# Performance work log

Hardware: AMD Instinct MI355X
Metric: run time of the kernel (lower is better)

## Reference

```python
import jax, jax.numpy as jnp
import numpy as np

B, H, K, V = 64, 32, 128, 128


def setup_inputs() -> dict:
    key = jax.random.key(0)
    ks = jax.random.split(key, 7)
    q = jax.random.normal(ks[0], (B, 1, H, K), dtype=jnp.float32)
    k = jax.random.normal(ks[1], (B, 1, H, K), dtype=jnp.float32)
    v = jax.random.normal(ks[2], (B, 1, H, V), dtype=jnp.float32)
    # a = -kappa, b = kappa*a_gate in RWKV-7; plain gaussians suffice for a math reference
    a = jax.random.normal(ks[3], (B, 1, H, K), dtype=jnp.float32)
    b = jax.random.normal(ks[4], (B, 1, H, K), dtype=jnp.float32)
    # gk is a log-decay: negative so exp(gk) in (0, 1]
    gk = -jnp.abs(jax.random.normal(ks[5], (B, 1, H, K), dtype=jnp.float32)) * 0.1
    h0 = jax.random.normal(ks[6], (B, H, K, V), dtype=jnp.float32) * 0.1
    return {"q": q, "k": k, "v": v, "a": a, "b": b, "gk": gk, "h0": h0}


def reference(q, k, v, a, b, gk, h0):
    """RWKV-7 DPLR single-step (T=1) decode recurrence, per (batch, head):
      g     = exp(gk)                                # [K] decay
      s     = a^T H0                                 # [V]
      t     = (q*g)^T H0                             # [V]
      alpha = q . b ; beta = q . k                   # scalars
      o     = t + alpha*s + beta*v                   # [V]
      Ht    = diag(g) H0 + b s^T + k v^T             # [K,V]
    Mirrors dplr_decode_t1_kernel_streamK exactly (fp32 accumulation).
    """
    qf = q[:, 0].astype(jnp.float32)   # [B,H,K]
    kf = k[:, 0].astype(jnp.float32)
    af = a[:, 0].astype(jnp.float32)
    bf = b[:, 0].astype(jnp.float32)
    vf = v[:, 0].astype(jnp.float32)   # [B,H,V]
    g = jnp.exp(gk[:, 0].astype(jnp.float32))  # [B,H,K]
    hf = h0.astype(jnp.float32)        # [B,H,K,V]

    s = jnp.einsum('bhk,bhkv->bhv', af, hf)
    t = jnp.einsum('bhk,bhkv->bhv', qf * g, hf)
    alpha = jnp.sum(qf * bf, axis=-1, keepdims=True)  # [B,H,1]
    beta = jnp.sum(qf * kf, axis=-1, keepdims=True)   # [B,H,1]
    o = t + alpha * s + beta * vf                      # [B,H,V]

    ht = g[..., None] * hf + bf[..., None] * s[:, :, None, :] + kf[..., None] * vf[:, :, None, :]
    return o[:, None].astype(v.dtype), ht.astype(h0.dtype)
```

## Files before the change

kernel.cpp:

```cpp
#include <hip/hip_runtime.h>


#define KD 128
#define VD 128
#define BH_TOTAL 2048
#define NGRP 16
#define RPT 8

typedef float f32x4 __attribute__((ext_vector_type(4)));

__global__ __launch_bounds__(512, 4) void dplr_decode_t1_kernel(
    const float* __restrict__ q_,  const float* __restrict__ k_,
    const float* __restrict__ v_,  const float* __restrict__ a_,
    const float* __restrict__ b_,  const float* __restrict__ gk_,
    const float* __restrict__ h0_, float* __restrict__ out_)
{
    const int bh  = blockIdx.x;
    const int tid = threadIdx.x;
    const int c4  = (tid & 31) * 4;
    const int grp = tid >> 5;
    const int r0  = grp * RPT;

    const size_t vec_off = (size_t)bh * KD;
    const size_t h_off   = (size_t)bh * (KD * VD);

    __shared__ float qs[KD], ks[KD], bs[KD], as_[KD], gs[KD], qgs[KD], vs[VD];
    __shared__ float sred[NGRP][VD];
    __shared__ float tred[NGRP][VD];
    __shared__ float red2[2];

    f32x4 Hreg[RPT];
    const float* hp = h0_ + h_off + (size_t)r0 * VD + c4;
#pragma unroll
    for (int j = 0; j < RPT; ++j) {
        Hreg[j] = *(const f32x4*)(hp + (size_t)j * VD);
    }

    const f32x4 v4 = *(const f32x4*)(v_ + vec_off + c4);

    if (tid < KD) {
        float qq = q_[vec_off + tid];
        float gg = expf(gk_[vec_off + tid]);
        qs[tid]  = qq;
        ks[tid]  = k_[vec_off + tid];
        bs[tid]  = b_[vec_off + tid];
        as_[tid] = a_[vec_off + tid];
        gs[tid]  = gg;
        qgs[tid] = qq * gg;
        vs[tid]  = v_[vec_off + tid];
    }

#pragma unroll
    for (int j = 0; j < RPT; ++j) {
        asm volatile("" : "+v"(Hreg[j]));
    }
    __syncthreads();

    if (tid < 64) {
        float p = qs[tid] * bs[tid] + qs[tid + 64] * bs[tid + 64];
#pragma unroll
        for (int o = 32; o > 0; o >>= 1) p += __shfl_down(p, o, 64);
        if (tid == 0) red2[0] = p;
    } else if (tid < 128) {
        int l = tid - 64;
        float p = qs[l] * ks[l] + qs[l + 64] * ks[l + 64];
#pragma unroll
        for (int o = 32; o > 0; o >>= 1) p += __shfl_down(p, o, 64);
        if (l == 0) red2[1] = p;
    }

    f32x4 sp = {0.f, 0.f, 0.f, 0.f};
    f32x4 tp = {0.f, 0.f, 0.f, 0.f};
#pragma unroll
    for (int j = 0; j < RPT; ++j) {
        const float av = as_[r0 + j];
        const float qg = qgs[r0 + j];
        const f32x4 h = Hreg[j];
        sp += av * h;
        tp += qg * h;
    }
    *(f32x4*)&sred[grp][c4] = sp;
    *(f32x4*)&tred[grp][c4] = tp;
    __syncthreads();

    f32x4 s4 = {0.f, 0.f, 0.f, 0.f};
#pragma unroll
    for (int g = 0; g < NGRP; ++g) {
        s4 += *(const f32x4*)&sred[g][c4];
    }

    if (tid < VD) {
        float sc = 0.f, tc = 0.f;
#pragma unroll
        for (int g = 0; g < NGRP; ++g) { sc += sred[g][tid]; tc += tred[g][tid]; }
        out_[(size_t)bh * VD + tid] = tc + red2[0] * sc + red2[1] * vs[tid];
    }

    float* op = out_ + (size_t)BH_TOTAL * VD + h_off + (size_t)r0 * VD + c4;
#pragma unroll
    for (int j = 0; j < RPT; ++j) {
        const int r = r0 + j;
        const float gr = gs[r];
        const float br = bs[r];
        const float kr = ks[r];
        f32x4 o4 = gr * Hreg[j] + br * s4 + kr * v4;
        __builtin_nontemporal_store(o4, (f32x4*)(op + (size_t)j * VD));
    }
}

extern "C" void kernel_launch(void* const* d_in, const int* in_sizes, int n_in,
                              void* d_out, int out_size, void* d_ws, size_t ws_size,
                              hipStream_t stream) {
    const float* q  = (const float*)d_in[0];
    const float* k  = (const float*)d_in[1];
    const float* v  = (const float*)d_in[2];
    const float* a  = (const float*)d_in[3];
    const float* b  = (const float*)d_in[4];
    const float* gk = (const float*)d_in[5];
    const float* h0 = (const float*)d_in[6];
    float* out = (float*)d_out;

    dplr_decode_t1_kernel<<<BH_TOTAL, 512, 0, stream>>>(q, k, v, a, b, gk, h0, out);
}
```

Measured before the change: 254.3 us.

## Make blocks persistent over four heads with double-buffered H prefetch

The grid shrinks from one block per (batch, head) to 512 blocks, and each block processes four consecutive heads. The next head's H tile and vectors are loaded into a second register set and shared buffer while the current head is reduced and written, so global loads overlap with compute and stores. This trades lower block count and parallelism for latency hiding. It also doubles H register usage, which may pressure occupancy under launch_bounds(512,4).

```diff
diff --git a/kernel.cpp b/kernel.cpp
--- a/kernel.cpp
+++ b/kernel.cpp
@@ -6,8 +6,18 @@
 #define BH_TOTAL 2048
 #define NGRP 16
 #define RPT 8
+#define GRID 512
+#define ITERS 4
 
 typedef float f32x4 __attribute__((ext_vector_type(4)));
+
+#define LDS_BARRIER()                                      \
+    do {                                                   \
+        asm volatile("s_waitcnt lgkmcnt(0)" ::: "memory"); \
+        __builtin_amdgcn_s_barrier();                      \
+        __builtin_amdgcn_sched_barrier(0);                 \
+        asm volatile("" ::: "memory");                     \
+    } while (0)
 
 __global__ __launch_bounds__(512, 4) void dplr_decode_t1_kernel(
     const float* __restrict__ q_,  const float* __restrict__ k_,
@@ -15,97 +25,117 @@
     const float* __restrict__ b_,  const float* __restrict__ gk_,
     const float* __restrict__ h0_, float* __restrict__ out_)
 {
-    const int bh  = blockIdx.x;
     const int tid = threadIdx.x;
     const int c4  = (tid & 31) * 4;
     const int grp = tid >> 5;
     const int r0  = grp * RPT;
+    const int bh0 = blockIdx.x * ITERS;
 
-    const size_t vec_off = (size_t)bh * KD;
-    const size_t h_off   = (size_t)bh * (KD * VD);
-
-    __shared__ float qs[KD], ks[KD], bs[KD], as_[KD], gs[KD], qgs[KD], vs[VD];
+    __shared__ float qs[2][KD], ks[2][KD], bs[2][KD], as_[2][KD],
+                     gs[2][KD], qgs[2][KD], vs[2][KD];
     __shared__ float sred[NGRP][VD];
     __shared__ float tred[NGRP][VD];
     __shared__ float red2[2];
 
-    f32x4 Hreg[RPT];
-    const float* hp = h0_ + h_off + (size_t)r0 * VD + c4;
-#pragma unroll
-    for (int j = 0; j < RPT; ++j) {
-        Hreg[j] = *(const f32x4*)(hp + (size_t)j * VD);
-    }
+    f32x4 Ha[RPT], Hb[RPT];
 
-    const f32x4 v4 = *(const f32x4*)(v_ + vec_off + c4);
+    float sq = 0.f, sk = 0.f, sb = 0.f, sa = 0.f, sg = 0.f, sv = 0.f;
 
-    if (tid < KD) {
-        float qq = q_[vec_off + tid];
-        float gg = expf(gk_[vec_off + tid]);
-        qs[tid]  = qq;
-        ks[tid]  = k_[vec_off + tid];
-        bs[tid]  = b_[vec_off + tid];
-        as_[tid] = a_[vec_off + tid];
-        gs[tid]  = gg;
-        qgs[tid] = qq * gg;
-        vs[tid]  = v_[vec_off + tid];
-    }
+#define STAGE_LOAD(bh)                                   \
+    do { if (tid < KD) {                                 \
+        const size_t off = (size_t)(bh)*KD + tid;        \
+        sq = q_[off];  sk = k_[off];  sb = b_[off];      \
+        sa = a_[off];  sg = gk_[off]; sv = v_[off];      \
+    } } while (0)
 
-#pragma unroll
-    for (int j = 0; j < RPT; ++j) {
-        asm volatile("" : "+v"(Hreg[j]));
-    }
-    __syncthreads();
+#define STAGE_WRITE(p)                                   \
+    do { if (tid < KD) {                                 \
+        const float gg = expf(sg);                       \
+        qs[p][tid]  = sq;  ks[p][tid] = sk;              \
+        bs[p][tid]  = sb;  as_[p][tid] = sa;             \
+        gs[p][tid]  = gg;  qgs[p][tid] = sq * gg;        \
+        vs[p][tid]  = sv;                                \
+    } } while (0)
 
-    if (tid < 64) {
-        float p = qs[tid] * bs[tid] + qs[tid + 64] * bs[tid + 64];
-#pragma unroll
-        for (int o = 32; o > 0; o >>= 1) p += __shfl_down(p, o, 64);
-        if (tid == 0) red2[0] = p;
-    } else if (tid < 128) {
-        int l = tid - 64;
-        float p = qs[l] * ks[l] + qs[l + 64] * ks[l + 64];
-#pragma unroll
-        for (int o = 32; o > 0; o >>= 1) p += __shfl_down(p, o, 64);
-        if (l == 0) red2[1] = p;
-    }
+#define LOAD_H(H, bh)                                                     \
+    do {                                                                  \
+        const float* hp_ = h0_ + (size_t)(bh)*(KD*VD) + (size_t)r0*VD + c4; \
+        _Pragma("unroll")                                                 \
+        for (int j = 0; j < RPT; ++j)                                     \
+            H[j] = *(const f32x4*)(hp_ + (size_t)j * VD);                 \
+    } while (0)
 
-    f32x4 sp = {0.f, 0.f, 0.f, 0.f};
-    f32x4 tp = {0.f, 0.f, 0.f, 0.f};
-#pragma unroll
-    for (int j = 0; j < RPT; ++j) {
-        const float av = as_[r0 + j];
-        const float qg = qgs[r0 + j];
-        const f32x4 h = Hreg[j];
-        sp += av * h;
-        tp += qg * h;
-    }
-    *(f32x4*)&sred[grp][c4] = sp;
-    *(f32x4*)&tred[grp][c4] = tp;
-    __syncthreads();
+    STAGE_LOAD(bh0);
+    STAGE_WRITE(0);
+    LOAD_H(Ha, bh0);
+    LDS_BARRIER();
 
-    f32x4 s4 = {0.f, 0.f, 0.f, 0.f};
-#pragma unroll
-    for (int g = 0; g < NGRP; ++g) {
-        s4 += *(const f32x4*)&sred[g][c4];
-    }
+#define ITER_BODY(i, HCUR, HNXT)                                              \
+    do {                                                                      \
+        const int p = (i) & 1;                                                \
+           \
+        if ((i) + 1 < ITERS) STAGE_LOAD(bh0 + (i) + 1);                       \
+                               \
+        if (tid < 64) {                                                       \
+            float pr = qs[p][tid]*bs[p][tid] + qs[p][tid+64]*bs[p][tid+64];   \
+            _Pragma("unroll")                                                 \
+            for (int o = 32; o > 0; o >>= 1) pr += __shfl_down(pr, o, 64);    \
+            if (tid == 0) red2[0] = pr;                                       \
+        } else if (tid < 128) {                                               \
+            const int l = tid - 64;                                           \
+            float pr = qs[p][l]*ks[p][l] + qs[p][l+64]*ks[p][l+64];           \
+            _Pragma("unroll")                                                 \
+            for (int o = 32; o > 0; o >>= 1) pr += __shfl_down(pr, o, 64);    \
+            if (l == 0) red2[1] = pr;                                         \
+        }                                                                     \
+                                              \
+        f32x4 sp = {0.f,0.f,0.f,0.f}, tp = {0.f,0.f,0.f,0.f};                 \
+        _Pragma("unroll")                                                     \
+        for (int j = 0; j < RPT; ++j) {                                       \
+            const float av = as_[p][r0+j];                                    \
+            const float qg = qgs[p][r0+j];                                    \
+            sp += av * HCUR[j];                                               \
+            tp += qg * HCUR[j];                                               \
+        }                                                                     \
+        *(f32x4*)&sred[grp][c4] = sp;                                         \
+        *(f32x4*)&tred[grp][c4] = tp;                                         \
+          \
+        if ((i) + 1 < ITERS) {                                                \
+            STAGE_WRITE(p ^ 1);                                               \
+            LOAD_H(HNXT, bh0 + (i) + 1);                                      \
+        }                                                                     \
+        LDS_BARRIER();       \
+                 \
+        f32x4 s4 = {0.f,0.f,0.f,0.f};                                         \
+        _Pragma("unroll")                                                     \
+        for (int g = 0; g < NGRP; ++g) s4 += *(const f32x4*)&sred[g][c4];     \
+        const f32x4 v4 = *(const f32x4*)&vs[p][c4];                           \
+        float* op = out_ + (size_t)BH_TOTAL * VD                              \
+                  + (size_t)(bh0+(i))*(KD*VD) + (size_t)r0*VD + c4;           \
+        _Pragma("unroll")                                                     \
+        for (int j = 0; j < RPT; ++j) {                                       \
+            const int r = r0 + j;                                             \
+            f32x4 o4 = gs[p][r]*HCUR[j] + bs[p][r]*s4 + ks[p][r]*v4;          \
+            __builtin_nontemporal_store(o4, (f32x4*)(op + (size_t)j*VD));     \
+        }                                                                     \
+        if (tid < VD) {                                                       \
+            float sc = 0.f, tc = 0.f;                                         \
+            _Pragma("unroll")                                                 \
+            for (int g = 0; g < NGRP; ++g) { sc += sred[g][tid]; tc += tred[g][tid]; } \
+            out_[(size_t)(bh0+(i))*VD + tid] = tc + red2[0]*sc + red2[1]*vs[p][tid];   \
+        }                                                                     \
+        LDS_BARRIER();           \
+    } while (0)
 
-    if (tid < VD) {
-        float sc = 0.f, tc = 0.f;
-#pragma unroll
-        for (int g = 0; g < NGRP; ++g) { sc += sred[g][tid]; tc += tred[g][tid]; }
-        out_[(size_t)bh * VD + tid] = tc + red2[0] * sc + red2[1] * vs[tid];
-    }
+    ITER_BODY(0, Ha, Hb);
+    ITER_BODY(1, Hb, Ha);
+    ITER_BODY(2, Ha, Hb);
+    ITER_BODY(3, Hb, Ha);
 
-    float* op = out_ + (size_t)BH_TOTAL * VD + h_off + (size_t)r0 * VD + c4;
-#pragma unroll
-    for (int j = 0; j < RPT; ++j) {
-        const int r = r0 + j;
-        const float gr = gs[r];
-        const float br = bs[r];
-        const float kr = ks[r];
-        f32x4 o4 = gr * Hreg[j] + br * s4 + kr * v4;
-        __builtin_nontemporal_store(o4, (f32x4*)(op + (size_t)j * VD));
-    }
+#undef ITER_BODY
+#undef LOAD_H
+#undef STAGE_WRITE
+#undef STAGE_LOAD
 }
 
 extern "C" void kernel_launch(void* const* d_in, const int* in_sizes, int n_in,
@@ -120,5 +150,5 @@
     const float* h0 = (const float*)d_in[6];
     float* out = (float*)d_out;
 
-    dplr_decode_t1_kernel<<<BH_TOTAL, 512, 0, stream>>>(q, k, v, a, b, gk, h0, out);
+    dplr_decode_t1_kernel<<<GRID, 512, 0, stream>>>(q, k, v, a, b, gk, h0, out);
 }
```

New measurement: 251.6 us. Within noise of the previous version (-1.1%).

## Split fused decode into separate reduce and update kernels via workspace

Applied to the files above, without the earlier changes.

Replaces the single fused kernel with two kernels when a workspace is available. The first computes s, t and the output vector and writes s to the workspace. The second rereads H0 and writes the updated state. This removes the need to hold H in registers across a block-wide reduction and barrier, but H0 (128 MiB) is now read twice and a second launch is added. The fused kernel remains as a fallback when no workspace is provided.

```diff
diff --git a/kernel.cpp b/kernel.cpp
--- a/kernel.cpp
+++ b/kernel.cpp
@@ -4,12 +4,115 @@
 #define KD 128
 #define VD 128
 #define BH_TOTAL 2048
-#define NGRP 16
-#define RPT 8
 
 typedef float f32x4 __attribute__((ext_vector_type(4)));
 
-__global__ __launch_bounds__(512, 4) void dplr_decode_t1_kernel(
+__global__ __launch_bounds__(256) void dplr_reduce_kernel(
+    const float* __restrict__ q_,  const float* __restrict__ k_,
+    const float* __restrict__ v_,  const float* __restrict__ a_,
+    const float* __restrict__ b_,  const float* __restrict__ gk_,
+    const float* __restrict__ h0_, float* __restrict__ out_,
+    float* __restrict__ s_ws)
+{
+    const int bh  = blockIdx.x;
+    const int tid = threadIdx.x;
+    const int c4  = (tid & 31) * 4;
+    const int grp = tid >> 5;
+    const int r0  = grp * 16;
+    const size_t vec_off = (size_t)bh * KD;
+
+    __shared__ float qs[KD], ks[KD], bs[KD], as_[KD], qgs[KD];
+    __shared__ float sred[8][VD], tred[8][VD];
+    __shared__ float red2[2];
+
+    float vv = 0.f;
+    if (tid < KD) {
+        const float qq = q_[vec_off + tid];
+        const float gg = expf(gk_[vec_off + tid]);
+        qs[tid]  = qq;
+        ks[tid]  = k_[vec_off + tid];
+        bs[tid]  = b_[vec_off + tid];
+        as_[tid] = a_[vec_off + tid];
+        qgs[tid] = qq * gg;
+        vv       = v_[vec_off + tid];
+    }
+    __syncthreads();
+
+    if (tid < 64) {
+        float p = qs[tid] * bs[tid] + qs[tid + 64] * bs[tid + 64];
+#pragma unroll
+        for (int o = 32; o > 0; o >>= 1) p += __shfl_down(p, o, 64);
+        if (tid == 0) red2[0] = p;
+    } else if (tid < 128) {
+        const int l = tid - 64;
+        float p = qs[l] * ks[l] + qs[l + 64] * ks[l + 64];
+#pragma unroll
+        for (int o = 32; o > 0; o >>= 1) p += __shfl_down(p, o, 64);
+        if (l == 0) red2[1] = p;
+    }
+
+    f32x4 sp = {0.f, 0.f, 0.f, 0.f};
+    f32x4 tp = {0.f, 0.f, 0.f, 0.f};
+    const float* hp = h0_ + (size_t)bh * (KD * VD) + (size_t)r0 * VD + c4;
+#pragma unroll
+    for (int j = 0; j < 16; ++j) {
+        const f32x4 h = *(const f32x4*)(hp + (size_t)j * VD);
+        sp += as_[r0 + j] * h;
+        tp += qgs[r0 + j] * h;
+    }
+    *(f32x4*)&sred[grp][c4] = sp;
+    *(f32x4*)&tred[grp][c4] = tp;
+    __syncthreads();
+
+    if (tid < VD) {
+        float sc = 0.f, tc = 0.f;
+#pragma unroll
+        for (int g = 0; g < 8; ++g) { sc += sred[g][tid]; tc += tred[g][tid]; }
+        out_[(size_t)bh * VD + tid] = tc + red2[0] * sc + red2[1] * vv;
+        s_ws[(size_t)bh * VD + tid] = sc;
+    }
+}
+
+__global__ __launch_bounds__(256) void dplr_update_kernel(
+    const float* __restrict__ k_,  const float* __restrict__ v_,
+    const float* __restrict__ b_,  const float* __restrict__ gk_,
+    const float* __restrict__ h0_, const float* __restrict__ s_ws,
+    float* __restrict__ out_)
+{
+    const int bh  = blockIdx.x;
+    const int tid = threadIdx.x;
+    const int c4  = (tid & 31) * 4;
+    const int grp = tid >> 5;
+    const int r0  = grp * 16;
+    const size_t vec_off = (size_t)bh * KD;
+
+    __shared__ float ks[KD], bs[KD], gs[KD], vs[KD], ss[KD];
+
+    if (tid < KD) {
+        ks[tid] = k_[vec_off + tid];
+        bs[tid] = b_[vec_off + tid];
+        gs[tid] = expf(gk_[vec_off + tid]);
+        vs[tid] = v_[vec_off + tid];
+        ss[tid] = s_ws[vec_off + tid];
+    }
+    __syncthreads();
+
+    const f32x4 s4 = *(const f32x4*)&ss[c4];
+    const f32x4 v4 = *(const f32x4*)&vs[c4];
+    const float* hp = h0_ + (size_t)bh * (KD * VD) + (size_t)r0 * VD + c4;
+    float* op = out_ + (size_t)BH_TOTAL * VD
+              + (size_t)bh * (KD * VD) + (size_t)r0 * VD + c4;
+
+#pragma unroll
+    for (int j = 0; j < 16; ++j) {
+        const int r = r0 + j;
+        const f32x4 h = *(const f32x4*)(hp + (size_t)j * VD);
+        f32x4 o4 = gs[r] * h + bs[r] * s4 + ks[r] * v4;
+        __builtin_nontemporal_store(o4, (f32x4*)(op + (size_t)j * VD));
+    }
+}
+
+__global__ __launch_bounds__(512, 4) void dplr_fused_kernel(
     const float* __restrict__ q_,  const float* __restrict__ k_,
     const float* __restrict__ v_,  const float* __restrict__ a_,
     const float* __restrict__ b_,  const float* __restrict__ gk_,
@@ -19,41 +122,32 @@
     const int tid = threadIdx.x;
     const int c4  = (tid & 31) * 4;
     const int grp = tid >> 5;
-    const int r0  = grp * RPT;
+    const int r0  = grp * 8;
 
     const size_t vec_off = (size_t)bh * KD;
     const size_t h_off   = (size_t)bh * (KD * VD);
 
-    __shared__ float qs[KD], ks[KD], bs[KD], as_[KD], gs[KD], qgs[KD], vs[VD];
-    __shared__ float sred[NGRP][VD];
-    __shared__ float tred[NGRP][VD];
+    __shared__ float qs[KD], ks[KD], bs[KD], as_[KD], gs[KD], qgs[KD], vs[KD];
+    __shared__ float sred[16][VD];
+    __shared__ float tred[16][VD];
     __shared__ float red2[2];
 
-    f32x4 Hreg[RPT];
+    f32x4 Hreg[8];
     const float* hp = h0_ + h_off + (size_t)r0 * VD + c4;
 #pragma unroll
-    for (int j = 0; j < RPT; ++j) {
-        Hreg[j] = *(const f32x4*)(hp + (size_t)j * VD);
-    }
+    for (int j = 0; j < 8; ++j) Hreg[j] = *(const f32x4*)(hp + (size_t)j * VD);
 
     const f32x4 v4 = *(const f32x4*)(v_ + vec_off + c4);
 
     if (tid < KD) {
         float qq = q_[vec_off + tid];
         float gg = expf(gk_[vec_off + tid]);
-        qs[tid]  = qq;
-        ks[tid]  = k_[vec_off + tid];
-        bs[tid]  = b_[vec_off + tid];
-        as_[tid] = a_[vec_off + tid];
-        gs[tid]  = gg;
-        qgs[tid] = qq * gg;
-        vs[tid]  = v_[vec_off + tid];
-    }
-
-#pragma unroll
-    for (int j = 0; j < RPT; ++j) {
-        asm volatile("" : "+v"(Hreg[j]));
-    }
+        qs[tid]  = qq;  ks[tid]  = k_[vec_off + tid];
+        bs[tid]  = b_[vec_off + tid];  as_[tid] = a_[vec_off + tid];
+        gs[tid]  = gg;  qgs[tid] = qq * gg;  vs[tid] = v_[vec_off + tid];
+    }
+#pragma unroll
+    for (int j = 0; j < 8; ++j) asm volatile("" : "+v"(Hreg[j]));
     __syncthreads();
 
     if (tid < 64) {
@@ -69,41 +163,32 @@
         if (l == 0) red2[1] = p;
     }
 
-    f32x4 sp = {0.f, 0.f, 0.f, 0.f};
-    f32x4 tp = {0.f, 0.f, 0.f, 0.f};
-#pragma unroll
-    for (int j = 0; j < RPT; ++j) {
-        const float av = as_[r0 + j];
-        const float qg = qgs[r0 + j];
-        const f32x4 h = Hreg[j];
-        sp += av * h;
-        tp += qg * h;
+    f32x4 sp = {0.f,0.f,0.f,0.f}, tp = {0.f,0.f,0.f,0.f};
+#pragma unroll
+    for (int j = 0; j < 8; ++j) {
+        sp += as_[r0 + j] * Hreg[j];
+        tp += qgs[r0 + j] * Hreg[j];
     }
     *(f32x4*)&sred[grp][c4] = sp;
     *(f32x4*)&tred[grp][c4] = tp;
     __syncthreads();
 
-    f32x4 s4 = {0.f, 0.f, 0.f, 0.f};
-#pragma unroll
-    for (int g = 0; g < NGRP; ++g) {
-        s4 += *(const f32x4*)&sred[g][c4];
-    }
+    f32x4 s4 = {0.f,0.f,0.f,0.f};
+#pragma unroll
+    for (int g = 0; g < 16; ++g) s4 += *(const f32x4*)&sred[g][c4];
 
     if (tid < VD) {
         float sc = 0.f, tc = 0.f;
 #pragma unroll
-        for (int g = 0; g < NGRP; ++g) { sc += sred[g][tid]; tc += tred[g][tid]; }
-        out_[(size_t)bh * VD + tid] = tc + red2[0] * sc + red2[1] * vs[tid];
+        for (int g = 0; g < 16; ++g) { sc += sred[g][tid]; tc += tred[g][tid]; }
+        out_[(size_t)bh * VD + tid] = tc + red2[0]*sc + red2[1]*vs[tid];
     }
 
     float* op = out_ + (size_t)BH_TOTAL * VD + h_off + (size_t)r0 * VD + c4;
 #pragma unroll
-    for (int j = 0; j < RPT; ++j) {
+    for (int j = 0; j < 8; ++j) {
         const int r = r0 + j;
-        const float gr = gs[r];
-        const float br = bs[r];
-        const float kr = ks[r];
-        f32x4 o4 = gr * Hreg[j] + br * s4 + kr * v4;
+        f32x4 o4 = gs[r]*Hreg[j] + bs[r]*s4 + ks[r]*v4;
         __builtin_nontemporal_store(o4, (f32x4*)(op + (size_t)j * VD));
     }
 }
@@ -120,5 +205,12 @@
     const float* h0 = (const float*)d_in[6];
     float* out = (float*)d_out;
 
-    dplr_decode_t1_kernel<<<BH_TOTAL, 512, 0, stream>>>(q, k, v, a, b, gk, h0, out);
-}
+    const size_t need = (size_t)BH_TOTAL * VD * sizeof(float);
+    if (d_ws != nullptr && ws_size >= need) {
+        float* s_ws = (float*)d_ws;
+        dplr_reduce_kernel<<<BH_TOTAL, 256, 0, stream>>>(q, k, v, a, b, gk, h0, out, s_ws);
+        dplr_update_kernel<<<BH_TOTAL, 256, 0, stream>>>(k, v, b, gk, h0, s_ws, out);
+    } else {
+        dplr_fused_kernel<<<BH_TOTAL, 512, 0, stream>>>(q, k, v, a, b, gk, h0, out);
+    }
+}
```

New measurement: 264.4 us. 1.04x slower.

## Map each batch-head to one wavefront with partial register caching of state

Applied to the files above, without the earlier changes.

Restructures the decode kernel so each wavefront handles one (batch, head) pair, four per block. Reductions use wave shuffles instead of block-wide shared-memory reductions and syncs. Only a quarter of the state rows are held in registers. The rest are re-read from global memory for the update pass, which trades extra read traffic for fewer registers and no block barriers.

```diff
diff --git a/kernel.cpp b/kernel.cpp
--- a/kernel.cpp
+++ b/kernel.cpp
@@ -4,107 +4,117 @@
 #define KD 128
 #define VD 128
 #define BH_TOTAL 2048
-#define NGRP 16
-#define RPT 8
+#define WPB 4
+#define NBLK (BH_TOTAL/WPB)
+#define RKEEP 16
+#define NSTRM (64 - RKEEP)
 
 typedef float f32x4 __attribute__((ext_vector_type(4)));
 
-__global__ __launch_bounds__(512, 4) void dplr_decode_t1_kernel(
+__global__ __launch_bounds__(256, 2) void dplr_decode_wave_kernel(
     const float* __restrict__ q_,  const float* __restrict__ k_,
     const float* __restrict__ v_,  const float* __restrict__ a_,
     const float* __restrict__ b_,  const float* __restrict__ gk_,
     const float* __restrict__ h0_, float* __restrict__ out_)
 {
-    const int bh  = blockIdx.x;
-    const int tid = threadIdx.x;
-    const int c4  = (tid & 31) * 4;
-    const int grp = tid >> 5;
-    const int r0  = grp * RPT;
+    const int tid  = threadIdx.x;
+    const int wid  = tid >> 6;
+    const int lane = tid & 63;
+    const int bh   = blockIdx.x * WPB + wid;
+    const int half = lane >> 5;
+    const int c4   = (lane & 31) * 4;
 
     const size_t vec_off = (size_t)bh * KD;
     const size_t h_off   = (size_t)bh * (KD * VD);
 
-    __shared__ float qs[KD], ks[KD], bs[KD], as_[KD], gs[KD], qgs[KD], vs[VD];
-    __shared__ float sred[NGRP][VD];
-    __shared__ float tred[NGRP][VD];
-    __shared__ float red2[2];
+    __shared__ float aL[WPB][2][64], qgL[WPB][2][64], gL[WPB][2][64],
+                     bL[WPB][2][64], kL[WPB][2][64];
 
-    f32x4 Hreg[RPT];
-    const float* hp = h0_ + h_off + (size_t)r0 * VD + c4;
+    const float q_lo = q_[vec_off + lane],  q_hi = q_[vec_off + lane + 64];
+    const float b_lo = b_[vec_off + lane],  b_hi = b_[vec_off + lane + 64];
+    const float k_lo = k_[vec_off + lane],  k_hi = k_[vec_off + lane + 64];
+    const float a_lo = a_[vec_off + lane],  a_hi = a_[vec_off + lane + 64];
+    const float g_lo = expf(gk_[vec_off + lane]);
+    const float g_hi = expf(gk_[vec_off + lane + 64]);
+
+    {
+        const int p  = lane & 1;
+        const int m0 = lane >> 1;
+        aL [wid][p][m0] = a_lo;        aL [wid][p][m0 + 32] = a_hi;
+        qgL[wid][p][m0] = q_lo * g_lo; qgL[wid][p][m0 + 32] = q_hi * g_hi;
+        gL [wid][p][m0] = g_lo;        gL [wid][p][m0 + 32] = g_hi;
+        bL [wid][p][m0] = b_lo;        bL [wid][p][m0 + 32] = b_hi;
+        kL [wid][p][m0] = k_lo;        kL [wid][p][m0 + 32] = k_hi;
+    }
+
+    float alpha = q_lo * b_lo + q_hi * b_hi;
+    float beta  = q_lo * k_lo + q_hi * k_hi;
 #pragma unroll
-    for (int j = 0; j < RPT; ++j) {
-        Hreg[j] = *(const f32x4*)(hp + (size_t)j * VD);
+    for (int o = 32; o > 0; o >>= 1) {
+        alpha += __shfl_xor(alpha, o, 64);
+        beta  += __shfl_xor(beta,  o, 64);
     }
 
     const f32x4 v4 = *(const f32x4*)(v_ + vec_off + c4);
 
-    if (tid < KD) {
-        float qq = q_[vec_off + tid];
-        float gg = expf(gk_[vec_off + tid]);
-        qs[tid]  = qq;
-        ks[tid]  = k_[vec_off + tid];
-        bs[tid]  = b_[vec_off + tid];
-        as_[tid] = a_[vec_off + tid];
-        gs[tid]  = gg;
-        qgs[tid] = qq * gg;
-        vs[tid]  = v_[vec_off + tid];
-    }
-
-#pragma unroll
-    for (int j = 0; j < RPT; ++j) {
-        asm volatile("" : "+v"(Hreg[j]));
-    }
-    __syncthreads();
-
-    if (tid < 64) {
-        float p = qs[tid] * bs[tid] + qs[tid + 64] * bs[tid + 64];
-#pragma unroll
-        for (int o = 32; o > 0; o >>= 1) p += __shfl_down(p, o, 64);
-        if (tid == 0) red2[0] = p;
-    } else if (tid < 128) {
-        int l = tid - 64;
-        float p = qs[l] * ks[l] + qs[l + 64] * ks[l + 64];
-#pragma unroll
-        for (int o = 32; o > 0; o >>= 1) p += __shfl_down(p, o, 64);
-        if (l == 0) red2[1] = p;
-    }
+    const float* hp = h0_ + h_off + (size_t)half * VD + c4;
 
     f32x4 sp = {0.f, 0.f, 0.f, 0.f};
     f32x4 tp = {0.f, 0.f, 0.f, 0.f};
+    f32x4 Hk[RKEEP];
+
 #pragma unroll
-    for (int j = 0; j < RPT; ++j) {
-        const float av = as_[r0 + j];
-        const float qg = qgs[r0 + j];
-        const f32x4 h = Hreg[j];
-        sp += av * h;
-        tp += qg * h;
+    for (int mb = 0; mb < NSTRM / 4; ++mb) {
+        const f32x4 av = *(const f32x4*)&aL [wid][half][mb * 4];
+        const f32x4 qv = *(const f32x4*)&qgL[wid][half][mb * 4];
+#pragma unroll
+        for (int e = 0; e < 4; ++e) {
+            const int m = mb * 4 + e;
+            const f32x4 h = *(const f32x4*)(hp + (size_t)m * 256);
+            sp += av[e] * h;
+            tp += qv[e] * h;
+        }
     }
-    *(f32x4*)&sred[grp][c4] = sp;
-    *(f32x4*)&tred[grp][c4] = tp;
-    __syncthreads();
-
-    f32x4 s4 = {0.f, 0.f, 0.f, 0.f};
 #pragma unroll
-    for (int g = 0; g < NGRP; ++g) {
-        s4 += *(const f32x4*)&sred[g][c4];
+    for (int j = 0; j < RKEEP; ++j) {
+        const int m = NSTRM + j;
+        Hk[j] = *(const f32x4*)(hp + (size_t)m * 256);
+        sp += aL [wid][half][m] * Hk[j];
+        tp += qgL[wid][half][m] * Hk[j];
     }
 
-    if (tid < VD) {
-        float sc = 0.f, tc = 0.f;
+    f32x4 s4, t4;
 #pragma unroll
-        for (int g = 0; g < NGRP; ++g) { sc += sred[g][tid]; tc += tred[g][tid]; }
-        out_[(size_t)bh * VD + tid] = tc + red2[0] * sc + red2[1] * vs[tid];
+    for (int e = 0; e < 4; ++e) {
+        s4[e] = sp[e] + __shfl_xor(sp[e], 32, 64);
+        t4[e] = tp[e] + __shfl_xor(tp[e], 32, 64);
     }
 
-    float* op = out_ + (size_t)BH_TOTAL * VD + h_off + (size_t)r0 * VD + c4;
+    if (half == 0) {
+        const f32x4 o4 = t4 + alpha * s4 + beta * v4;
+        *(f32x4*)(out_ + (size_t)bh * VD + c4) = o4;
+    }
+
+    float* op = out_ + (size_t)BH_TOTAL * VD + h_off + (size_t)half * VD + c4;
 #pragma unroll
-    for (int j = 0; j < RPT; ++j) {
-        const int r = r0 + j;
-        const float gr = gs[r];
-        const float br = bs[r];
-        const float kr = ks[r];
-        f32x4 o4 = gr * Hreg[j] + br * s4 + kr * v4;
-        __builtin_nontemporal_store(o4, (f32x4*)(op + (size_t)j * VD));
+    for (int mb = 0; mb < NSTRM / 4; ++mb) {
+        const f32x4 gv = *(const f32x4*)&gL[wid][half][mb * 4];
+        const f32x4 bv = *(const f32x4*)&bL[wid][half][mb * 4];
+        const f32x4 kv = *(const f32x4*)&kL[wid][half][mb * 4];
+#pragma unroll
+        for (int e = 0; e < 4; ++e) {
+            const int m = mb * 4 + e;
+            const f32x4 h = __builtin_nontemporal_load((const f32x4*)(hp + (size_t)m * 256));
+            const f32x4 o4 = gv[e] * h + bv[e] * s4 + kv[e] * v4;
+            __builtin_nontemporal_store(o4, (f32x4*)(op + (size_t)m * 256));
+        }
+    }
+#pragma unroll
+    for (int j = 0; j < RKEEP; ++j) {
+        const int m = NSTRM + j;
+        const f32x4 o4 = gL[wid][half][m] * Hk[j] + bL[wid][half][m] * s4
+                       + kL[wid][half][m] * v4;
+        __builtin_nontemporal_store(o4, (f32x4*)(op + (size_t)m * 256));
     }
 }
 
@@ -120,5 +130,5 @@
     const float* h0 = (const float*)d_in[6];
     float* out = (float*)d_out;
 
-    dplr_decode_t1_kernel<<<BH_TOTAL, 512, 0, stream>>>(q, k, v, a, b, gk, h0, out);
+    dplr_decode_wave_kernel<<<NBLK, 256, 0, stream>>>(q, k, v, a, b, gk, h0, out);
 }
```

Measured after the change: 254.4 us. No clear change (+0.0%).
